# Performance work log

Hardware: AMD Instinct MI355X
Metric: run time of the kernel (lower is better)

The kernel has to match this reference:

```python
import jax, jax.numpy as jnp
import numpy as np

HIDDEN = 2048
HEADS = 16
HEAD_DIM = HIDDEN // HEADS
D_FF = 4 * HIDDEN
B, T = 2, 2048
LN_EPS = 1e-5


def setup_inputs() -> dict:
    key = jax.random.key(0)
    ks = jax.random.split(key, 12)
    s = 0.02
    x = jax.random.normal(ks[0], (B, T, HIDDEN), dtype=jnp.float32)
    # strict upper-triangular True == masked (causal)
    causal_mask = jnp.triu(jnp.ones((T, T), dtype=bool), k=1)
    # weights stored as [in, out] (equivalent to torch Linear weight.T)
    Wq = jax.random.normal(ks[1], (HIDDEN, HIDDEN), jnp.float32) * s
    Wk = jax.random.normal(ks[2], (HIDDEN, HIDDEN), jnp.float32) * s
    Wv = jax.random.normal(ks[3], (HIDDEN, HIDDEN), jnp.float32) * s
    Wo = jax.random.normal(ks[4], (HIDDEN, HIDDEN), jnp.float32) * s
    ln1_w = jnp.ones((HIDDEN,), jnp.float32)
    ln1_b = jnp.zeros((HIDDEN,), jnp.float32)
    ln2_w = jnp.ones((HIDDEN,), jnp.float32)
    ln2_b = jnp.zeros((HIDDEN,), jnp.float32)
    W1 = jax.random.normal(ks[5], (HIDDEN, D_FF), jnp.float32) * s
    b1 = jnp.zeros((D_FF,), jnp.float32)
    W2 = jax.random.normal(ks[6], (D_FF, HIDDEN), jnp.float32) * s
    b2 = jnp.zeros((HIDDEN,), jnp.float32)
    return dict(x=x, causal_mask=causal_mask, Wq=Wq, Wk=Wk, Wv=Wv, Wo=Wo,
                ln1_w=ln1_w, ln1_b=ln1_b, ln2_w=ln2_w, ln2_b=ln2_b,
                W1=W1, b1=b1, W2=W2, b2=b2)


def _layernorm(x, w, b):
    mu = jnp.mean(x, axis=-1, keepdims=True)
    var = jnp.mean(jnp.square(x - mu), axis=-1, keepdims=True)
    return (x - mu) * jax.lax.rsqrt(var + LN_EPS) * w + b


def reference(x, causal_mask, Wq, Wk, Wv, Wo, ln1_w, ln1_b, ln2_w, ln2_b, W1, b1, W2, b2):
    Bx, Tx, H = x.shape
    h = _layernorm(x, ln1_w, ln1_b)
    # [B, T, heads, head_dim] -> [B, heads, T, head_dim]
    q = (h @ Wq).reshape(Bx, Tx, HEADS, HEAD_DIM).transpose(0, 2, 1, 3)
    k = (h @ Wk).reshape(Bx, Tx, HEADS, HEAD_DIM).transpose(0, 2, 1, 3)
    v = (h @ Wv).reshape(Bx, Tx, HEADS, HEAD_DIM).transpose(0, 2, 1, 3)
    scale = 1.0 / jnp.sqrt(jnp.float32(HEAD_DIM))
    scores = jnp.einsum('bhqd,bhkd->bhqk', q, k) * scale  # [B, heads, T, T]
    scores = jnp.where(causal_mask, -jnp.inf, scores)
    attn = jax.nn.softmax(scores, axis=-1)
    out = jnp.einsum('bhqk,bhkd->bhqd', attn, v)  # [B, heads, T, head_dim]
    out = out.transpose(0, 2, 1, 3).reshape(Bx, Tx, H)
    x = x + out @ Wo
    h2 = _layernorm(x, ln2_w, ln2_b)
    mlp = jax.nn.silu(h2 @ W1 + b1) @ W2 + b2
    return x + mlp
```

## Files before the change

### kernel.cpp

```cpp
#include <hip/hip_runtime.h>

#define HID 2048
#define NH 16
#define DH 128
#define DFF 8192
#define BB 2
#define TT 2048
#define MROWS 4096

typedef __bf16 bf16x8 __attribute__((ext_vector_type(8)));
typedef __bf16 bf16x4 __attribute__((ext_vector_type(4)));
typedef float  f32x4  __attribute__((ext_vector_type(4)));

__device__ __forceinline__ f32x4 mfma16(bf16x8 a, bf16x8 b, f32x4 c) {
    return __builtin_amdgcn_mfma_f32_16x16x32_bf16(a, b, c, 0, 0, 0);
}

__device__ __forceinline__ void gload_lds16(const __bf16* gsrc, __bf16* ldst) {
    __builtin_amdgcn_global_load_lds(
        (const __attribute__((address_space(1))) void*)gsrc,
        (__attribute__((address_space(3))) void*)ldst, 16, 0, 0);
}

template<int K, int N>
__global__ __launch_bounds__(256) void transpose_bf16_kernel(
    const float* __restrict__ W, __bf16* __restrict__ Wt) {
    __shared__ float tile[64][65];
    int t = threadIdx.x;
    int n0 = blockIdx.x * 64, k0 = blockIdx.y * 64;
    int n4 = (t & 15) * 4, kk = t >> 4;
    #pragma unroll
    for (int i = 0; i < 4; i++) {
        int k = i * 16 + kk;
        float4 v = *(const float4*)(W + (size_t)(k0 + k) * N + n0 + n4);
        tile[k][n4] = v.x; tile[k][n4 + 1] = v.y;
        tile[k][n4 + 2] = v.z; tile[k][n4 + 3] = v.w;
    }
    __syncthreads();
    int k4 = (t & 15) * 4, nn = t >> 4;
    #pragma unroll
    for (int i = 0; i < 4; i++) {
        int n = i * 16 + nn;
        bf16x4 o;
        #pragma unroll
        for (int j = 0; j < 4; j++) o[j] = (__bf16)tile[k4 + j][n];
        *(bf16x4*)(Wt + (size_t)(n0 + n) * K + k0 + k4) = o;
    }
}

__global__ __launch_bounds__(256) void ln_kernel(
    const float* __restrict__ x, const float* __restrict__ gw,
    const float* __restrict__ gb, __bf16* __restrict__ out) {
    int row = blockIdx.x;
    int t = threadIdx.x;
    const float* xr = x + (size_t)row * HID;
    float4 v0 = *(const float4*)(xr + t * 8);
    float4 v1 = *(const float4*)(xr + t * 8 + 4);
    float xv[8] = {v0.x, v0.y, v0.z, v0.w, v1.x, v1.y, v1.z, v1.w};
    float s = 0.f, q = 0.f;
    #pragma unroll
    for (int j = 0; j < 8; j++) { s += xv[j]; q += xv[j] * xv[j]; }
    #pragma unroll
    for (int off = 1; off < 64; off <<= 1) {
        s += __shfl_xor(s, off);
        q += __shfl_xor(q, off);
    }
    __shared__ float ssum[4], ssq[4];
    if ((t & 63) == 0) { ssum[t >> 6] = s; ssq[t >> 6] = q; }
    __syncthreads();
    s = ssum[0] + ssum[1] + ssum[2] + ssum[3];
    q = ssq[0] + ssq[1] + ssq[2] + ssq[3];
    float mu = s * (1.0f / HID);
    float var = q * (1.0f / HID) - mu * mu;
    float rs = rsqrtf(var + 1e-5f);
    bf16x8 o;
    #pragma unroll
    for (int j = 0; j < 8; j++)
        o[j] = (__bf16)((xv[j] - mu) * rs * gw[t * 8 + j] + gb[t * 8 + j]);
    *(bf16x8*)(out + (size_t)row * HID + t * 8) = o;
}

template<int EPI, int BN, int BK, int N, int K>
__global__ __launch_bounds__(512) void gemm8(
    const __bf16* __restrict__ A, const __bf16* __restrict__ Bt,
    void* __restrict__ C0, void* __restrict__ C1, void* __restrict__ C2,
    const float* __restrict__ resid, const float* __restrict__ bias, int nN) {
    constexpr int BM = 256;
    constexpr int CPR = BK / 8;
    constexpr int RND_A = BM * BK * 2 / 8192;
    constexpr int RND_B = BN * BK * 2 / 8192;
    constexpr int LPT = RND_A + RND_B;
    constexpr int NT = K / BK;
    constexpr int WC = BN / 4;
    constexpr int NFRAG = WC / 16;
    constexpr int KK = BK / 32;

    __shared__ __align__(16) __bf16 As[3][BM * BK];
    __shared__ __align__(16) __bf16 Bs[3][BN * BK];

    int tid = threadIdx.x;
    int w = tid >> 6, l = tid & 63;
    int wr = w >> 2, wc = w & 3;
    int qi = l & 15, g = l >> 4;

    int nwg = gridDim.x;
    int bid = blockIdx.x;
    int wg = (bid & 7) * (nwg >> 3) + (bid >> 3);
    int bm = wg / nN, bn = wg % nN;
    int row0 = bm * BM, col0 = bn * BN;

    const __bf16* pA[RND_A];
    #pragma unroll
    for (int i = 0; i < RND_A; i++) {
        int slot = i * 512 + tid;
        int r = slot / CPR, u = slot % CPR;
        pA[i] = A + (size_t)(row0 + r) * K + (u ^ (r & (CPR - 1))) * 8;
    }
    const __bf16* pB[RND_B];
    #pragma unroll
    for (int i = 0; i < RND_B; i++) {
        int slot = i * 512 + tid;
        int r = slot / CPR, u = slot % CPR;
        pB[i] = Bt + (size_t)(col0 + r) * K + (u ^ (r & (CPR - 1))) * 8;
    }
    int wbase = w * 64 * 8;

    f32x4 acc[8][NFRAG] = {};

    #pragma unroll
    for (int tt = 0; tt < 2; tt++) {
        #pragma unroll
        for (int i = 0; i < RND_A; i++)
            gload_lds16(pA[i] + tt * BK, &As[tt][i * 4096 + wbase]);
        #pragma unroll
        for (int i = 0; i < RND_B; i++)
            gload_lds16(pB[i] + tt * BK, &Bs[tt][i * 4096 + wbase]);
    }

    __bf16 *a0 = As[0], *a1 = As[1], *a2 = As[2];
    __bf16 *b0 = Bs[0], *b1 = Bs[1], *b2 = Bs[2];

    for (int t = 0; t < NT; t++) {
        if constexpr (LPT == 6) asm volatile("s_waitcnt vmcnt(6)" ::: "memory");
        else                    asm volatile("s_waitcnt vmcnt(4)" ::: "memory");
        __builtin_amdgcn_s_barrier();
        asm volatile("" ::: "memory");
        if (t + 2 < NT) {
            #pragma unroll
            for (int i = 0; i < RND_A; i++)
                gload_lds16(pA[i] + (t + 2) * BK, a2 + i * 4096 + wbase);
            #pragma unroll
            for (int i = 0; i < RND_B; i++)
                gload_lds16(pB[i] + (t + 2) * BK, b2 + i * 4096 + wbase);
        }
        bf16x8 af[8][KK], bfr[NFRAG][KK];
        #pragma unroll
        for (int m = 0; m < 8; m++) {
            int r = wr * 128 + m * 16 + qi;
            #pragma unroll
            for (int kk = 0; kk < KK; kk++) {
                int byt = r * (BK * 2) + ((kk * 64 + g * 16) ^ ((r & (CPR - 1)) << 4));
                af[m][kk] = *(const bf16x8*)((const char*)a0 + byt);
            }
        }
        #pragma unroll
        for (int n = 0; n < NFRAG; n++) {
            int r = wc * WC + n * 16 + qi;
            #pragma unroll
            for (int kk = 0; kk < KK; kk++) {
                int byt = r * (BK * 2) + ((kk * 64 + g * 16) ^ ((r & (CPR - 1)) << 4));
                bfr[n][kk] = *(const bf16x8*)((const char*)b0 + byt);
            }
        }
        __builtin_amdgcn_s_setprio(1);
        #pragma unroll
        for (int kk = 0; kk < KK; kk++)
            #pragma unroll
            for (int m = 0; m < 8; m++)
                #pragma unroll
                for (int n = 0; n < NFRAG; n++)
                    acc[m][n] = mfma16(af[m][kk], bfr[n][kk], acc[m][n]);
        __builtin_amdgcn_s_setprio(0);
        asm volatile("" ::: "memory");
        __bf16* ta = a0; a0 = a1; a1 = a2; a2 = ta;
        __bf16* tb = b0; b0 = b1; b1 = b2; b2 = tb;
    }

    #pragma unroll
    for (int m = 0; m < 8; m++) {
        #pragma unroll
        for (int n = 0; n < NFRAG; n++) {
            int Rb = row0 + wr * 128 + m * 16 + g * 4;
            int C = col0 + wc * WC + n * 16 + qi;
            if constexpr (EPI == 6) {
                int region = C >> 11;
                int Cl = C & 2047;
                if (region < 2) {
                    __bf16* dst = (__bf16*)(region == 0 ? C0 : C1);
                    #pragma unroll
                    for (int r = 0; r < 4; r++)
                        dst[(size_t)(Rb + r) * 2048 + Cl] = (__bf16)acc[m][n][r];
                } else {
                    bf16x4 pk;
                    #pragma unroll
                    for (int r = 0; r < 4; r++) pk[r] = (__bf16)acc[m][n][r];
                    int b = Rb >> 11, t0 = Rb & 2047, hh = Cl >> 7, d = Cl & 127;
                    *(bf16x4*)((__bf16*)C2 + ((size_t)(b * NH + hh) * DH + d) * TT + t0) = pk;
                }
            } else {
                #pragma unroll
                for (int r = 0; r < 4; r++) {
                    int R = Rb + r;
                    float v = acc[m][n][r];
                    size_t idx = (size_t)R * N + C;
                    if constexpr (EPI == 0) {
                        ((__bf16*)C0)[idx] = (__bf16)v;
                    } else if constexpr (EPI == 2) {
                        ((float*)C0)[idx] = resid[idx] + v;
                    } else if constexpr (EPI == 3) {
                        float u = v + bias[C];
                        ((__bf16*)C0)[idx] = (__bf16)(u / (1.f + __expf(-u)));
                    } else if constexpr (EPI == 4) {
                        float u = v + bias[C];
                        ((float*)C0)[idx] = resid[idx] + u;
                    }
                }
            }
        }
    }
}

__global__ __launch_bounds__(256) void attn_kernel(
    const __bf16* __restrict__ qh, const __bf16* __restrict__ kh,
    const __bf16* __restrict__ vt, __bf16* __restrict__ out) {
    __shared__ __align__(16) __bf16 Ks[64 * 128];
    __shared__ __align__(16) __bf16 Vts[128 * 64];
    __shared__ __align__(16) __bf16 plds[4][1024];
    int tid = threadIdx.x;
    int w = tid >> 6, l = tid & 63;
    int qi = l & 15, g = l >> 4;
    int bh = blockIdx.y;
    int b = bh >> 4, hd = bh & 15;
    int qtile = gridDim.x - 1 - blockIdx.x;
    int qbase = qtile * 64 + w * 16;
    int qg = qbase + qi;

    const __bf16* qrow = qh + ((size_t)b * TT + qg) * HID + hd * DH;
    const __bf16* kbase = kh + (size_t)b * TT * HID + hd * DH;
    const __bf16* vtb = vt + (size_t)bh * DH * TT;

    bf16x8 bq[4];
    #pragma unroll
    for (int kc = 0; kc < 4; kc++)
        bq[kc] = *(const bf16x8*)(qrow + kc * 32 + g * 8);

    f32x4 O[8] = {};
    float m_run = -3.0e38f, l_run = 0.f;
    const float scale = 0.08838834764831845f;
    int nt = qtile + 1;

    for (int it = 0; it < nt; it++) {
        int kv0 = it * 64;
        __syncthreads();
        #pragma unroll
        for (int i = 0; i < 4; i++) {
            int j = (w * 4 + i) * 64 + l;
            int r = j >> 4, u = j & 15;
            int cb = (u * 16) ^ ((r & 7) << 4);
            gload_lds16(kbase + (size_t)(kv0 + r) * HID + (cb >> 1),
                        Ks + (w * 4 + i) * 512);
        }
        #pragma unroll
        for (int i = 0; i < 4; i++) {
            int j = (w * 4 + i) * 64 + l;
            int r = j >> 3, u = j & 7;
            int cb = (u * 16) ^ ((r & 7) << 4);
            gload_lds16(vtb + (size_t)r * TT + kv0 + (cb >> 1),
                        Vts + (w * 4 + i) * 512);
        }
        __syncthreads();

        f32x4 st[4] = {};
        __builtin_amdgcn_s_setprio(1);
        #pragma unroll
        for (int t = 0; t < 4; t++) {
            #pragma unroll
            for (int kc = 0; kc < 4; kc++) {
                int row = t * 16 + qi;
                int cb = (kc * 64 + g * 16) ^ ((qi & 7) << 4);
                bf16x8 ak = *(const bf16x8*)(Ks + row * 128 + (cb >> 1));
                st[t] = mfma16(ak, bq[kc], st[t]);
            }
        }
        __builtin_amdgcn_s_setprio(0);
        float s[16];
        #pragma unroll
        for (int t = 0; t < 4; t++)
            #pragma unroll
            for (int r = 0; r < 4; r++) s[t * 4 + r] = st[t][r] * scale;
        #pragma unroll
        for (int i = 0; i < 16; i++) {
            int kvg = kv0 + (i >> 2) * 16 + g * 4 + (i & 3);
            if (kvg > qg) s[i] = -3.0e38f;
        }
        float mt = s[0];
        #pragma unroll
        for (int i = 1; i < 16; i++) mt = fmaxf(mt, s[i]);
        mt = fmaxf(mt, __shfl_xor(mt, 16));
        mt = fmaxf(mt, __shfl_xor(mt, 32));
        float m_new = fmaxf(m_run, mt);
        float alpha = __expf(m_run - m_new);
        float p[16], ps = 0.f;
        #pragma unroll
        for (int i = 0; i < 16; i++) { p[i] = __expf(s[i] - m_new); ps += p[i]; }
        ps += __shfl_xor(ps, 16);
        ps += __shfl_xor(ps, 32);
        l_run = l_run * alpha + ps;
        m_run = m_new;

        #pragma unroll
        for (int t = 0; t < 4; t++) {
            bf16x4 pk;
            #pragma unroll
            for (int r = 0; r < 4; r++) pk[r] = (__bf16)p[t * 4 + r];
            int cb = (t * 32 + g * 8) ^ ((qi & 7) << 4);
            *(bf16x4*)(&plds[w][qi * 64 + (cb >> 1)]) = pk;
        }

        float av[4];
        #pragma unroll
        for (int r = 0; r < 4; r++) av[r] = __shfl(alpha, (g << 4) | (g * 4 + r));
        #pragma unroll
        for (int oc = 0; oc < 8; oc++)
            #pragma unroll
            for (int r = 0; r < 4; r++) O[oc][r] *= av[r];

        #pragma unroll
        for (int h = 0; h < 2; h++) {
            int cbp = (h * 64 + g * 16) ^ ((qi & 7) << 4);
            bf16x8 ap = *(const bf16x8*)(&plds[w][qi * 64 + (cbp >> 1)]);
            __builtin_amdgcn_s_setprio(1);
            #pragma unroll
            for (int oc = 0; oc < 8; oc++) {
                int row = oc * 16 + qi;
                int cb = (h * 64 + g * 16) ^ ((qi & 7) << 4);
                bf16x8 bv = *(const bf16x8*)(Vts + row * 64 + (cb >> 1));
                O[oc] = mfma16(ap, bv, O[oc]);
            }
            __builtin_amdgcn_s_setprio(0);
        }
    }

    float linv[4];
    #pragma unroll
    for (int r = 0; r < 4; r++) {
        float lq = __shfl(l_run, (g << 4) | (g * 4 + r));
        linv[r] = 1.0f / lq;
    }
    __bf16* op = out + ((size_t)b * TT + qbase) * HID + hd * DH;
    #pragma unroll
    for (int oc = 0; oc < 8; oc++)
        #pragma unroll
        for (int r = 0; r < 4; r++)
            op[(size_t)(g * 4 + r) * HID + oc * 16 + qi] = (__bf16)(O[oc][r] * linv[r]);
}

extern "C" void kernel_launch(void* const* d_in, const int* in_sizes, int n_in,
                              void* d_out, int out_size, void* d_ws, size_t ws_size,
                              hipStream_t stream) {
    const float* x    = (const float*)d_in[0];
    const float* Wq   = (const float*)d_in[2];
    const float* Wk   = (const float*)d_in[3];
    const float* Wv   = (const float*)d_in[4];
    const float* Wo   = (const float*)d_in[5];
    const float* ln1w = (const float*)d_in[6];
    const float* ln1b = (const float*)d_in[7];
    const float* ln2w = (const float*)d_in[8];
    const float* ln2b = (const float*)d_in[9];
    const float* W1   = (const float*)d_in[10];
    const float* b1   = (const float*)d_in[11];
    const float* W2   = (const float*)d_in[12];
    const float* b2   = (const float*)d_in[13];
    float* outp = (float*)d_out;

    char* ws = (char*)d_ws;
    const size_t SZ_W   = (size_t)HID * HID * 2;
    const size_t SZ_WF  = (size_t)HID * DFF * 2;
    const size_t SZ_ACT = (size_t)MROWS * HID * 2;
    const size_t SZ_X32 = (size_t)MROWS * HID * 4;

    __bf16* wqT  = (__bf16*)(ws);
    __bf16* wkT  = (__bf16*)(ws + SZ_W);
    __bf16* wvT  = (__bf16*)(ws + 2 * SZ_W);
    __bf16* woT  = (__bf16*)(ws + 3 * SZ_W);
    __bf16* w1T  = (__bf16*)(ws + 4 * SZ_W);
    __bf16* w2T  = (__bf16*)(ws + 4 * SZ_W + SZ_WF);
    __bf16* h    = (__bf16*)(ws + 4 * SZ_W + 2 * SZ_WF);
    float*  x1   = (float*) (ws + 4 * SZ_W + 2 * SZ_WF + SZ_ACT);
    char*   base = ws + 4 * SZ_W + 2 * SZ_WF + SZ_ACT + SZ_X32;
    __bf16* qb   = (__bf16*)(base);
    __bf16* kb   = (__bf16*)(base + SZ_ACT);
    __bf16* vtb  = (__bf16*)(base + 2 * SZ_ACT);
    __bf16* attn = (__bf16*)(base + 3 * SZ_ACT);
    __bf16* mlp1 = (__bf16*)(base);

    dim3 blk256(256), blk512(512);
    transpose_bf16_kernel<HID, HID><<<dim3(32, 32), blk256, 0, stream>>>(Wq, wqT);
    transpose_bf16_kernel<HID, HID><<<dim3(32, 32), blk256, 0, stream>>>(Wk, wkT);
    transpose_bf16_kernel<HID, HID><<<dim3(32, 32), blk256, 0, stream>>>(Wv, wvT);
    transpose_bf16_kernel<HID, HID><<<dim3(32, 32), blk256, 0, stream>>>(Wo, woT);
    transpose_bf16_kernel<HID, DFF><<<dim3(128, 32), blk256, 0, stream>>>(W1, w1T);
    transpose_bf16_kernel<DFF, HID><<<dim3(32, 128), blk256, 0, stream>>>(W2, w2T);

    ln_kernel<<<MROWS, blk256, 0, stream>>>(x, ln1w, ln1b, h);

    gemm8<6, 256, 32, 6144, HID><<<384, blk512, 0, stream>>>(
        h, wqT, qb, kb, vtb, nullptr, nullptr, 24);

    attn_kernel<<<dim3(TT / 64, BB * NH), blk256, 0, stream>>>(qb, kb, vtb, attn);

    gemm8<2, 128, 64, HID, HID><<<256, blk512, 0, stream>>>(
        attn, woT, x1, nullptr, nullptr, x, nullptr, 16);

    ln_kernel<<<MROWS, blk256, 0, stream>>>(x1, ln2w, ln2b, h);

    gemm8<3, 256, 32, DFF, HID><<<512, blk512, 0, stream>>>(
        h, w1T, mlp1, nullptr, nullptr, nullptr, b1, 32);

    gemm8<4, 128, 64, HID, DFF><<<256, blk512, 0, stream>>>(
        mlp1, w2T, outp, nullptr, nullptr, x1, b2, 16);
}
```

Baseline: 773.6 us.

## Double-buffer K/V tiles in attention and batch four weight transposes

The attention kernel now keeps two LDS buffers for the K and V^T tiles and issues the async global-to-LDS loads for the next KV tile before computing on the current one. Partial vmcnt waits and raw barriers replace the two full __syncthreads per iteration. Separately, the four square weight transposes are merged into one launch using blockIdx.z. The double buffering doubles the K/V LDS footprint, which may lower occupancy. It also relies on the vmcnt(8) count matching the eight loads issued per stage.

After: 777.4 us. No clear change (+0.5%).

```diff
diff --git a/kernel.cpp b/kernel.cpp
--- a/kernel.cpp
+++ b/kernel.cpp
@@ -23,11 +23,10 @@
 }
 
 template<int K, int N>
-__global__ __launch_bounds__(256) void transpose_bf16_kernel(
-    const float* __restrict__ W, __bf16* __restrict__ Wt) {
-    __shared__ float tile[64][65];
-    int t = threadIdx.x;
-    int n0 = blockIdx.x * 64, k0 = blockIdx.y * 64;
+__device__ __forceinline__ void transpose_tile(
+    const float* __restrict__ W, __bf16* __restrict__ Wt,
+    int bx, int by, int t, float (*tile)[65]) {
+    int n0 = bx * 64, k0 = by * 64;
     int n4 = (t & 15) * 4, kk = t >> 4;
     #pragma unroll
     for (int i = 0; i < 4; i++) {
@@ -46,6 +45,25 @@
         for (int j = 0; j < 4; j++) o[j] = (__bf16)tile[k4 + j][n];
         *(bf16x4*)(Wt + (size_t)(n0 + n) * K + k0 + k4) = o;
     }
+}
+
+template<int K, int N>
+__global__ __launch_bounds__(256) void transpose_bf16_kernel(
+    const float* __restrict__ W, __bf16* __restrict__ Wt) {
+    __shared__ float tile[64][65];
+    transpose_tile<K, N>(W, Wt, blockIdx.x, blockIdx.y, threadIdx.x, tile);
+}
+
+__global__ __launch_bounds__(256) void transpose4_kernel(
+    const float* __restrict__ W0, const float* __restrict__ W1,
+    const float* __restrict__ W2, const float* __restrict__ W3,
+    __bf16* __restrict__ D0, __bf16* __restrict__ D1,
+    __bf16* __restrict__ D2, __bf16* __restrict__ D3) {
+    __shared__ float tile[64][65];
+    int z = blockIdx.z;
+    const float* W = (z == 0) ? W0 : (z == 1) ? W1 : (z == 2) ? W2 : W3;
+    __bf16* D = (z == 0) ? D0 : (z == 1) ? D1 : (z == 2) ? D2 : D3;
+    transpose_tile<HID, HID>(W, D, blockIdx.x, blockIdx.y, threadIdx.x, tile);
 }
 
 __global__ __launch_bounds__(256) void ln_kernel(
@@ -233,8 +251,8 @@
 __global__ __launch_bounds__(256) void attn_kernel(
     const __bf16* __restrict__ qh, const __bf16* __restrict__ kh,
     const __bf16* __restrict__ vt, __bf16* __restrict__ out) {
-    __shared__ __align__(16) __bf16 Ks[64 * 128];
-    __shared__ __align__(16) __bf16 Vts[128 * 64];
+    __shared__ __align__(16) __bf16 Ks[2][64 * 128];
+    __shared__ __align__(16) __bf16 Vts[2][128 * 64];
     __shared__ __align__(16) __bf16 plds[4][1024];
     int tid = threadIdx.x;
     int w = tid >> 6, l = tid & 63;
@@ -254,21 +272,15 @@
     for (int kc = 0; kc < 4; kc++)
         bq[kc] = *(const bf16x8*)(qrow + kc * 32 + g * 8);
 
-    f32x4 O[8] = {};
-    float m_run = -3.0e38f, l_run = 0.f;
-    const float scale = 0.08838834764831845f;
-    int nt = qtile + 1;
-
-    for (int it = 0; it < nt; it++) {
+    auto stage = [&](int it, int sb) {
         int kv0 = it * 64;
-        __syncthreads();
         #pragma unroll
         for (int i = 0; i < 4; i++) {
             int j = (w * 4 + i) * 64 + l;
             int r = j >> 4, u = j & 15;
             int cb = (u * 16) ^ ((r & 7) << 4);
             gload_lds16(kbase + (size_t)(kv0 + r) * HID + (cb >> 1),
-                        Ks + (w * 4 + i) * 512);
+                        Ks[sb] + (w * 4 + i) * 512);
         }
         #pragma unroll
         for (int i = 0; i < 4; i++) {
@@ -276,9 +288,26 @@
             int r = j >> 3, u = j & 7;
             int cb = (u * 16) ^ ((r & 7) << 4);
             gload_lds16(vtb + (size_t)r * TT + kv0 + (cb >> 1),
-                        Vts + (w * 4 + i) * 512);
-        }
-        __syncthreads();
+                        Vts[sb] + (w * 4 + i) * 512);
+        }
+    };
+
+    f32x4 O[8] = {};
+    float m_run = -3.0e38f, l_run = 0.f;
+    const float scale = 0.08838834764831845f;
+    int nt = qtile + 1;
+
+    stage(0, 0);
+    for (int it = 0; it < nt; it++) {
+        int cur = it & 1;
+        int kv0 = it * 64;
+        if (it + 1 < nt) {
+            stage(it + 1, cur ^ 1);
+            asm volatile("s_waitcnt vmcnt(8)" ::: "memory");
+        } else {
+            asm volatile("s_waitcnt vmcnt(0)" ::: "memory");
+        }
+        __builtin_amdgcn_s_barrier();
 
         f32x4 st[4] = {};
         __builtin_amdgcn_s_setprio(1);
@@ -288,7 +317,7 @@
             for (int kc = 0; kc < 4; kc++) {
                 int row = t * 16 + qi;
                 int cb = (kc * 64 + g * 16) ^ ((qi & 7) << 4);
-                bf16x8 ak = *(const bf16x8*)(Ks + row * 128 + (cb >> 1));
+                bf16x8 ak = *(const bf16x8*)(Ks[cur] + row * 128 + (cb >> 1));
                 st[t] = mfma16(ak, bq[kc], st[t]);
             }
         }
@@ -344,11 +373,12 @@
             for (int oc = 0; oc < 8; oc++) {
                 int row = oc * 16 + qi;
                 int cb = (h * 64 + g * 16) ^ ((qi & 7) << 4);
-                bf16x8 bv = *(const bf16x8*)(Vts + row * 64 + (cb >> 1));
+                bf16x8 bv = *(const bf16x8*)(Vts[cur] + row * 64 + (cb >> 1));
                 O[oc] = mfma16(ap, bv, O[oc]);
             }
             __builtin_amdgcn_s_setprio(0);
         }
+        __builtin_amdgcn_s_barrier();
     }
 
     float linv[4];
@@ -405,10 +435,8 @@
     __bf16* mlp1 = (__bf16*)(base);
 
     dim3 blk256(256), blk512(512);
-    transpose_bf16_kernel<HID, HID><<<dim3(32, 32), blk256, 0, stream>>>(Wq, wqT);
-    transpose_bf16_kernel<HID, HID><<<dim3(32, 32), blk256, 0, stream>>>(Wk, wkT);
-    transpose_bf16_kernel<HID, HID><<<dim3(32, 32), blk256, 0, stream>>>(Wv, wvT);
-    transpose_bf16_kernel<HID, HID><<<dim3(32, 32), blk256, 0, stream>>>(Wo, woT);
+    transpose4_kernel<<<dim3(32, 32, 4), blk256, 0, stream>>>(
+        Wq, Wk, Wv, Wo, wqT, wkT, wvT, woT);
     transpose_bf16_kernel<HID, DFF><<<dim3(128, 32), blk256, 0, stream>>>(W1, w1T);
     transpose_bf16_kernel<DFF, HID><<<dim3(32, 128), blk256, 0, stream>>>(W2, w2T);
 
```
